# Performance work log

Hardware: AMD Instinct MI355X
Metric: run time of the kernel (lower is better)

## Reference

```python
import jax, jax.numpy as jnp
import numpy as np

D_MODEL = 1024
NUM_HEADS = 16

def setup_inputs() -> dict:
    key = jax.random.key(0)
    ks = jax.random.split(key, 9)
    d = D_MODEL
    s = 0.02
    return {
        "x": jax.random.normal(ks[0], (2, 2048, d), dtype=jnp.float32),
        "wq": jax.random.normal(ks[1], (d, d), dtype=jnp.float32) * s,
        "bq": jax.random.normal(ks[2], (d,), dtype=jnp.float32) * s,
        "wk": jax.random.normal(ks[3], (d, d), dtype=jnp.float32) * s,
        "bk": jax.random.normal(ks[4], (d,), dtype=jnp.float32) * s,
        "wv": jax.random.normal(ks[5], (d, d), dtype=jnp.float32) * s,
        "bv": jax.random.normal(ks[6], (d,), dtype=jnp.float32) * s,
        "wo": jax.random.normal(ks[7], (d, d), dtype=jnp.float32) * s,
        "bo": jax.random.normal(ks[8], (d,), dtype=jnp.float32) * s,
    }

def reference(x, wq, bq, wk, bk, wv, bv, wo, bo) -> jnp.ndarray:
    b, s, d = x.shape
    h = NUM_HEADS
    dk = d // h
    # projections (torch Linear: x @ W^T + b)
    q = x @ wq.T + bq
    k = x @ wk.T + bk
    v = x @ wv.T + bv
    # split heads -> [b, h, s, dk]
    q = q.reshape(b, s, h, dk).transpose(0, 2, 1, 3)
    k = k.reshape(b, s, h, dk).transpose(0, 2, 1, 3)
    v = v.reshape(b, s, h, dk).transpose(0, 2, 1, 3)
    scale = jnp.sqrt(jnp.asarray(dk, dtype=x.dtype))
    scores = jnp.einsum('bhqd,bhkd->bhqk', q, k) / scale
    causal = jnp.tril(jnp.ones((s, s), dtype=bool))  # [s, s]
    scores = jnp.where(causal[None, None], scores, jnp.asarray(-jnp.inf, dtype=x.dtype))
    attn = jax.nn.softmax(scores, axis=-1)
    out = jnp.einsum('bhqk,bhkd->bhqd', attn, v)
    out = out.transpose(0, 2, 1, 3).reshape(b, s, d)
    return out @ wo.T + bo
```

## Files before the change

### kernel.cpp

```cpp
#include <hip/hip_runtime.h>

#define D_MODEL 1024
#define NHEAD   16
#define DK      64
#define BATCH   2
#define SEQ     2048
#define M_TOT   (BATCH*SEQ)

typedef unsigned short u16;
typedef unsigned int   u32;
typedef __attribute__((ext_vector_type(8))) __bf16 bf16x8;
typedef __attribute__((ext_vector_type(8))) u16   u16x8;
typedef __attribute__((ext_vector_type(4))) u16   u16x4;
typedef __attribute__((ext_vector_type(4))) float f32x4;

typedef const __attribute__((address_space(1))) u32* gas_ptr;
typedef __attribute__((address_space(3))) u32*       las_ptr;

__device__ __forceinline__ void gload16(const u16* g, u16* l) {
  __builtin_amdgcn_global_load_lds((gas_ptr)g, (las_ptr)l, 16, 0, 0);
}

__device__ __forceinline__ u16 bfc(float f) {
  union { __bf16 h; u16 u; } v; v.h = (__bf16)f; return v.u;
}

#define BAR() do { \
  __builtin_amdgcn_sched_barrier(0); \
  __builtin_amdgcn_s_barrier(); \
  __builtin_amdgcn_sched_barrier(0); \
} while (0)

__global__ void cvt_all(const float* __restrict__ x,
                        const float* __restrict__ wq, const float* __restrict__ wk,
                        const float* __restrict__ wv, const float* __restrict__ wo,
                        u16* __restrict__ xbf, u16* __restrict__ wbf) {
  const int y = blockIdx.y;
  const float* src;
  u16* dst;
  int n8;
  if (y == 0)      { src = x;  dst = xbf;                n8 = M_TOT * D_MODEL / 8; }
  else if (y == 1) { src = wq; dst = wbf;                n8 = 1024 * 1024 / 8; }
  else if (y == 2) { src = wk; dst = wbf + 1 * 1048576;  n8 = 1024 * 1024 / 8; }
  else if (y == 3) { src = wv; dst = wbf + 2 * 1048576;  n8 = 1024 * 1024 / 8; }
  else             { src = wo; dst = wbf + 3 * 1048576;  n8 = 1024 * 1024 / 8; }
  for (int i = blockIdx.x * blockDim.x + threadIdx.x; i < n8; i += gridDim.x * blockDim.x) {
    const float4* s = (const float4*)src + (size_t)i * 2;
    float4 a = s[0], b = s[1];
    u16x8 o;
    o[0]=bfc(a.x); o[1]=bfc(a.y); o[2]=bfc(a.z); o[3]=bfc(a.w);
    o[4]=bfc(b.x); o[5]=bfc(b.y); o[6]=bfc(b.z); o[7]=bfc(b.w);
    *((u16x8*)dst + i) = o;
  }
}

#define QSCALE 0.18033688011112042f

__global__ __launch_bounds__(256) void qkv_gemm(
    const u16* __restrict__ xbf, const u16* __restrict__ wbf,
    const float* __restrict__ bq, const float* __restrict__ bk, const float* __restrict__ bv,
    u16* __restrict__ qws, u16* __restrict__ kws, u16* __restrict__ vtws)
{
  __shared__ u16 la[2 * 128 * 32];
  __shared__ u16 lb[2 * 64 * 32];
  const int z     = blockIdx.z;
  const int nbase = blockIdx.x * 64;
  const int mbase = blockIdx.y * 128;
  const u16*  A    = xbf;
  const u16*  Bm   = wbf + (size_t)z * 1024 * 1024;
  const float* bias = (z == 0) ? bq : (z == 1) ? bk : bv;

  const int tid  = threadIdx.x;
  const int lane = tid & 63;
  const int wid  = tid >> 6;
  const int wr   = (wid >> 1) * 64, wc = (wid & 1) * 32;
  const int lr   = lane & 15, lg = lane >> 4;
  const int srow = tid >> 2;
  const int sc   = tid & 3;
  const int sdst = srow * 32 + sc * 8;
  const int ssrc = (sc ^ ((srow >> 1) & 3)) * 8;
  const int csw  = (lg ^ ((lr >> 1) & 3)) * 8;

  f32x4 acc[4][2];
  #pragma unroll
  for (int i = 0; i < 4; ++i) { acc[i][0] = (f32x4){0,0,0,0}; acc[i][1] = (f32x4){0,0,0,0}; }

  #define STAGEQ(u, bi) do { \
    const int k0_ = (u) * 32; \
    gload16(&A [(size_t)(mbase + srow)      * 1024 + k0_ + ssrc], &la[(bi)*4096 + sdst]); \
    gload16(&A [(size_t)(mbase + srow + 64) * 1024 + k0_ + ssrc], &la[(bi)*4096 + 64*32 + sdst]); \
    gload16(&Bm[(size_t)(nbase + srow)      * 1024 + k0_ + ssrc], &lb[(bi)*2048 + sdst]); \
  } while (0)

  STAGEQ(0, 0);
  STAGEQ(1, 1);
  for (int t = 0; t < 32; ++t) {
    if (t < 31) asm volatile("s_waitcnt vmcnt(3)" ::: "memory");
    else        asm volatile("s_waitcnt vmcnt(0)" ::: "memory");
    BAR();
    const int cb = (t & 1) * 4096, cbb = (t & 1) * 2048;
    bf16x8 af[4], bfr[2];
    #pragma unroll
    for (int i = 0; i < 4; ++i)
      af[i] = *(const bf16x8*)&la[cb + (wr + i*16 + lr)*32 + csw];
    #pragma unroll
    for (int j = 0; j < 2; ++j)
      bfr[j] = *(const bf16x8*)&lb[cbb + (wc + j*16 + lr)*32 + csw];
    #pragma unroll
    for (int i = 0; i < 4; ++i)
      #pragma unroll
      for (int j = 0; j < 2; ++j)
        acc[i][j] = __builtin_amdgcn_mfma_f32_16x16x32_bf16(af[i], bfr[j], acc[i][j], 0, 0, 0);
    BAR();
    if (t + 2 < 32) STAGEQ(t + 2, t & 1);
  }
  #undef STAGEQ

  #pragma unroll
  for (int i = 0; i < 4; ++i) {
    #pragma unroll
    for (int j = 0; j < 2; ++j) {
      int gn = nbase + wc + j*16 + lr;
      float bs = bias[gn];
      int h = gn >> 6, d = gn & 63;
      int gm0 = mbase + wr + i*16 + lg*4;
      int bb = gm0 >> 11, s0 = gm0 & 2047;
      if (z == 2) {
        u16x4 vk;
        #pragma unroll
        for (int r = 0; r < 4; ++r) vk[r] = bfc(acc[i][j][r] + bs);
        *(u16x4*)&vtws[(((size_t)(bb*NHEAD + h)) * DK + d) * SEQ + s0] = vk;
      } else {
        #pragma unroll
        for (int r = 0; r < 4; ++r) {
          float v = acc[i][j][r] + bs;
          if (z == 0) qws[(((size_t)(bb*NHEAD + h)) * SEQ + s0 + r) * DK + d] = bfc(v * QSCALE);
          else        kws[(((size_t)(bb*NHEAD + h)) * SEQ + s0 + r) * DK + d] = bfc(v);
        }
      }
    }
  }
}

__global__ __launch_bounds__(256) void out_gemm(
    const u16* __restrict__ ows, const u16* __restrict__ wobf,
    const float* __restrict__ bo, float* __restrict__ out)
{
  __shared__ u16 la[2 * 64 * 64];
  __shared__ u16 lb[2 * 64 * 64];
  const int nbase = blockIdx.x * 64;
  const int mbase = blockIdx.y * 64;
  const int tid  = threadIdx.x;
  const int lane = tid & 63;
  const int wid  = tid >> 6;
  const int wr   = (wid >> 1) * 32, wc = (wid & 1) * 32;
  const int lr   = lane & 15, lg = lane >> 4;
  const int srow = tid >> 3;
  const int sc   = tid & 7;
  const int sdst = srow * 64 + sc * 8;
  const int ssrc = (sc ^ (srow & 7)) * 8;
  const int lsw  = lr & 7;

  f32x4 acc[2][2];
  acc[0][0] = (f32x4){0,0,0,0}; acc[0][1] = (f32x4){0,0,0,0};
  acc[1][0] = (f32x4){0,0,0,0}; acc[1][1] = (f32x4){0,0,0,0};

  #define STAGEO(u, bi) do { \
    const int k0_ = (u) * 64; \
    gload16(&ows [(size_t)(mbase + srow)      * 1024 + k0_ + ssrc], &la[(bi)*4096 + sdst]); \
    gload16(&ows [(size_t)(mbase + srow + 32) * 1024 + k0_ + ssrc], &la[(bi)*4096 + 32*64 + sdst]); \
    gload16(&wobf[(size_t)(nbase + srow)      * 1024 + k0_ + ssrc], &lb[(bi)*4096 + sdst]); \
    gload16(&wobf[(size_t)(nbase + srow + 32) * 1024 + k0_ + ssrc], &lb[(bi)*4096 + 32*64 + sdst]); \
  } while (0)

  STAGEO(0, 0);
  STAGEO(1, 1);
  for (int t = 0; t < 16; ++t) {
    if (t < 15) asm volatile("s_waitcnt vmcnt(4)" ::: "memory");
    else        asm volatile("s_waitcnt vmcnt(0)" ::: "memory");
    BAR();
    const int cb = (t & 1) * 4096;
    bf16x8 af[2][2], bfr[2][2];
    #pragma unroll
    for (int kk = 0; kk < 2; ++kk) {
      #pragma unroll
      for (int i = 0; i < 2; ++i)
        af[i][kk] = *(const bf16x8*)&la[cb + (wr + i*16 + lr)*64 + (((kk*4 + lg) ^ lsw) * 8)];
      #pragma unroll
      for (int j = 0; j < 2; ++j)
        bfr[j][kk] = *(const bf16x8*)&lb[cb + (wc + j*16 + lr)*64 + (((kk*4 + lg) ^ lsw) * 8)];
    }
    #pragma unroll
    for (int kk = 0; kk < 2; ++kk)
      #pragma unroll
      for (int i = 0; i < 2; ++i)
        #pragma unroll
        for (int j = 0; j < 2; ++j)
          acc[i][j] = __builtin_amdgcn_mfma_f32_16x16x32_bf16(af[i][kk], bfr[j][kk], acc[i][j], 0, 0, 0);
    BAR();
    if (t + 2 < 16) STAGEO(t + 2, t & 1);
  }
  #undef STAGEO

  #pragma unroll
  for (int i = 0; i < 2; ++i) {
    #pragma unroll
    for (int j = 0; j < 2; ++j) {
      int gn = nbase + wc + j*16 + lr;
      float bs = bo[gn];
      #pragma unroll
      for (int r = 0; r < 4; ++r) {
        int gm = mbase + wr + i*16 + lg*4 + r;
        out[(size_t)gm * 1024 + gn] = acc[i][j][r] + bs;
      }
    }
  }
}

__global__ __launch_bounds__(256) void attn_kernel(
    const u16* __restrict__ qws, const u16* __restrict__ kws,
    const u16* __restrict__ vtws, u16* __restrict__ ows)
{
  __shared__ u16 kbuf[2 * 64 * 64];
  __shared__ u16 vbuf[2 * 64 * 64];
  __shared__ u16 pbuf[4 * 16 * 64];
  const int flat = blockIdx.x;
  const int r    = flat & 7;
  const int g    = flat >> 3;
  const int bh_l = g >> 5;
  const int qp   = g & 31;
  const int qt   = (bh_l & 1) ? qp : (31 - qp);
  const int bh   = r * 4 + bh_l;
  const int b = bh >> 4, h = bh & 15;
  const int tid = threadIdx.x, wid = tid >> 6, lane = tid & 63;
  const int lr = lane & 15, lg = lane >> 4;
  const u16* Q  = qws  + (size_t)(b * NHEAD + h) * SEQ * DK;
  const u16* K  = kws  + (size_t)(b * NHEAD + h) * SEQ * DK;
  const u16* Vt = vtws + (size_t)(b * NHEAD + h) * DK * SEQ;

  const int sr  = tid >> 3;
  const int sc8 = (tid & 7) * 8;
  const int c0s = ((tid & 7) ^ (sr & 7)) * 8;
  const int c1s = ((tid & 7) ^ ((sr + 32) & 7)) * 8;

  #define STAGE(u, bi) do { \
    const int kb_ = (u) * 64; \
    const int off_ = (bi) * 4096; \
    gload16(&K[(size_t)(kb_ + sr) * DK + c0s],        &kbuf[off_ + sr * 64 + sc8]); \
    gload16(&K[(size_t)(kb_ + sr + 32) * DK + c1s],   &kbuf[off_ + (sr + 32) * 64 + sc8]); \
    gload16(&Vt[(size_t)sr * SEQ + kb_ + c0s],        &vbuf[off_ + sr * 64 + sc8]); \
    gload16(&Vt[(size_t)(sr + 32) * SEQ + kb_ + c1s], &vbuf[off_ + (sr + 32) * 64 + sc8]); \
  } while (0)
  #define CH(m) ((((m)*4 + lg) ^ (lr & 7)) * 8)

  const int qbase  = qt * 64 + wid * 16;
  const int q_glob = qbase + lr;

  bf16x8 qf0 = *(const bf16x8*)&Q[(size_t)q_glob * DK + lg * 8];
  bf16x8 qf1 = *(const bf16x8*)&Q[(size_t)q_glob * DK + 32 + lg * 8];

  f32x4 oacc[4];
  #pragma unroll
  for (int t = 0; t < 4; ++t) oacc[t] = (f32x4){0.f, 0.f, 0.f, 0.f};
  float l_run = 0.f;

  STAGE(0, 0);
  if (qt >= 1) STAGE(1, 1);

  for (int t = 0; t <= qt; ++t) {
    if (t < qt) asm volatile("s_waitcnt vmcnt(4)" ::: "memory");
    else        asm volatile("s_waitcnt vmcnt(0)" ::: "memory");
    BAR();

    const int diag = (t == qt);
    const int nsub = diag ? (wid + 1) : 4;
    const int cb = (t & 1) * 4096;

    f32x4 sacc[4];
    __builtin_amdgcn_s_setprio(1);
    #pragma unroll
    for (int ts = 0; ts < 4; ++ts) {
      if (ts >= nsub) continue;
      bf16x8 kf0 = *(const bf16x8*)&kbuf[cb + (ts*16 + lr) * 64 + CH(0)];
      bf16x8 kf1 = *(const bf16x8*)&kbuf[cb + (ts*16 + lr) * 64 + CH(1)];
      f32x4 s0 = (f32x4){0.f, 0.f, 0.f, 0.f};
      s0 = __builtin_amdgcn_mfma_f32_16x16x32_bf16(kf0, qf0, s0, 0, 0, 0);
      s0 = __builtin_amdgcn_mfma_f32_16x16x32_bf16(kf1, qf1, s0, 0, 0, 0);
      sacc[ts] = s0;
    }
    __builtin_amdgcn_s_setprio(0);
    if (diag) {
      const int ts = wid;
      #pragma unroll
      for (int r2 = 0; r2 < 4; ++r2)
        if (lg * 4 + r2 > lr) sacc[ts][r2] = -1e30f;
    }
    #pragma unroll
    for (int ts = 0; ts < 4; ++ts) {
      if (ts >= nsub) continue;
      #pragma unroll
      for (int r2 = 0; r2 < 4; ++r2) {
        float p = __builtin_amdgcn_exp2f(sacc[ts][r2]);
        sacc[ts][r2] = p;
        l_run += p;
      }
    }

    #pragma unroll
    for (int ts = 0; ts < 4; ++ts) {
      u16x4 pk;
      if (ts < nsub) {
        pk[0] = bfc(sacc[ts][0]); pk[1] = bfc(sacc[ts][1]);
        pk[2] = bfc(sacc[ts][2]); pk[3] = bfc(sacc[ts][3]);
      } else {
        pk[0] = 0; pk[1] = 0; pk[2] = 0; pk[3] = 0;
      }
      const int pc = (((ts*2 + (lg >> 1)) ^ (lr & 7)) * 8) + (lg & 1) * 4;
      *(u16x4*)&pbuf[wid * 1024 + lr * 64 + pc] = pk;
    }
    asm volatile("s_waitcnt lgkmcnt(0)" ::: "memory");
    __builtin_amdgcn_sched_barrier(0);
    bf16x8 pf0 = *(const bf16x8*)&pbuf[wid * 1024 + lr * 64 + CH(0)];
    bf16x8 pf1 = *(const bf16x8*)&pbuf[wid * 1024 + lr * 64 + CH(1)];

    __builtin_amdgcn_s_setprio(1);
    #pragma unroll
    for (int td = 0; td < 4; ++td) {
      bf16x8 vf0 = *(const bf16x8*)&vbuf[cb + (td*16 + lr) * 64 + CH(0)];
      bf16x8 vf1 = *(const bf16x8*)&vbuf[cb + (td*16 + lr) * 64 + CH(1)];
      oacc[td] = __builtin_amdgcn_mfma_f32_16x16x32_bf16(vf0, pf0, oacc[td], 0, 0, 0);
      oacc[td] = __builtin_amdgcn_mfma_f32_16x16x32_bf16(vf1, pf1, oacc[td], 0, 0, 0);
    }
    __builtin_amdgcn_s_setprio(0);
    BAR();
    if (t + 2 <= qt) STAGE(t + 2, t & 1);
  }

  float l_tot = l_run;
  l_tot += __shfl_xor(l_tot, 16);
  l_tot += __shfl_xor(l_tot, 32);
  const float inv = 1.0f / l_tot;
  #pragma unroll
  for (int td = 0; td < 4; ++td) {
    u16x4 ok;
    #pragma unroll
    for (int r2 = 0; r2 < 4; ++r2) ok[r2] = bfc(oacc[td][r2] * inv);
    *(u16x4*)&ows[((size_t)(b * SEQ + q_glob)) * D_MODEL + h * DK + td*16 + lg*4] = ok;
  }
  #undef CH
  #undef STAGE
}

extern "C" void kernel_launch(void* const* d_in, const int* in_sizes, int n_in,
                              void* d_out, int out_size, void* d_ws, size_t ws_size,
                              hipStream_t stream) {
  const float* x  = (const float*)d_in[0];
  const float* wq = (const float*)d_in[1];
  const float* bq = (const float*)d_in[2];
  const float* wk = (const float*)d_in[3];
  const float* bk = (const float*)d_in[4];
  const float* wv = (const float*)d_in[5];
  const float* bv = (const float*)d_in[6];
  const float* wo = (const float*)d_in[7];
  const float* bo = (const float*)d_in[8];
  float* out = (float*)d_out;

  char* ws = (char*)d_ws;
  u16* qws  = (u16*)(ws + (size_t) 0 * (1 << 20));
  u16* kws  = (u16*)(ws + (size_t) 8 * (1 << 20));
  u16* vtws = (u16*)(ws + (size_t)16 * (1 << 20));
  u16* ows  = (u16*)(ws + (size_t)24 * (1 << 20));
  u16* xbf  = (u16*)(ws + (size_t)32 * (1 << 20));
  u16* wbf  = (u16*)(ws + (size_t)40 * (1 << 20));

  cvt_all<<<dim3(512, 5), 256, 0, stream>>>(x, wq, wk, wv, wo, xbf, wbf);

  qkv_gemm<<<dim3(1024 / 64, M_TOT / 128, 3), 256, 0, stream>>>(
      xbf, wbf, bq, bk, bv, qws, kws, vtws);

  attn_kernel<<<dim3(1024, 1, 1), 256, 0, stream>>>(qws, kws, vtws, ows);

  out_gemm<<<dim3(1024 / 64, M_TOT / 64), 256, 0, stream>>>(
      ows, wbf + (size_t)3 * 1024 * 1024, bo, out);
}
```

Before: 113.4 us.

## Shrink projection GEMM blocks to 64x64 with two waves and simpler double buffering

Both projection GEMMs now use 128-thread blocks computing 64x64 tiles, with each wave owning a 64x32 slab. The QKV GEMM grid doubles to 3072 blocks, and the output GEMM moves to BK=32 with 32 k-steps. The hand-tuned vmcnt waits and depth-2 prefetch are replaced by a simpler prefetch-next-then-syncthreads loop. The aim is more blocks and better occupancy, at the cost of more global traffic per FLOP in the QKV GEMM and loads that may not be fully waited on before __syncthreads.

```diff
diff --git a/kernel.cpp b/kernel.cpp
--- a/kernel.cpp
+++ b/kernel.cpp
@@ -56,16 +56,16 @@
 
 #define QSCALE 0.18033688011112042f
 
-__global__ __launch_bounds__(256) void qkv_gemm(
+__global__ __launch_bounds__(128) void qkv_gemm(
     const u16* __restrict__ xbf, const u16* __restrict__ wbf,
     const float* __restrict__ bq, const float* __restrict__ bk, const float* __restrict__ bv,
     u16* __restrict__ qws, u16* __restrict__ kws, u16* __restrict__ vtws)
 {
-  __shared__ u16 la[2 * 128 * 32];
+  __shared__ u16 la[2 * 64 * 32];
   __shared__ u16 lb[2 * 64 * 32];
   const int z     = blockIdx.z;
   const int nbase = blockIdx.x * 64;
-  const int mbase = blockIdx.y * 128;
+  const int mbase = blockIdx.y * 64;
   const u16*  A    = xbf;
   const u16*  Bm   = wbf + (size_t)z * 1024 * 1024;
   const float* bias = (z == 0) ? bq : (z == 1) ? bk : bv;
@@ -73,7 +73,7 @@
   const int tid  = threadIdx.x;
   const int lane = tid & 63;
   const int wid  = tid >> 6;
-  const int wr   = (wid >> 1) * 64, wc = (wid & 1) * 32;
+  const int wc   = wid * 32;
   const int lr   = lane & 15, lg = lane >> 4;
   const int srow = tid >> 2;
   const int sc   = tid & 3;
@@ -87,32 +87,32 @@
 
   #define STAGEQ(u, bi) do { \
     const int k0_ = (u) * 32; \
-    gload16(&A [(size_t)(mbase + srow)      * 1024 + k0_ + ssrc], &la[(bi)*4096 + sdst]); \
-    gload16(&A [(size_t)(mbase + srow + 64) * 1024 + k0_ + ssrc], &la[(bi)*4096 + 64*32 + sdst]); \
+    gload16(&A [(size_t)(mbase + srow)      * 1024 + k0_ + ssrc], &la[(bi)*2048 + sdst]); \
+    gload16(&A [(size_t)(mbase + srow + 32) * 1024 + k0_ + ssrc], &la[(bi)*2048 + 1024 + sdst]); \
     gload16(&Bm[(size_t)(nbase + srow)      * 1024 + k0_ + ssrc], &lb[(bi)*2048 + sdst]); \
+    gload16(&Bm[(size_t)(nbase + srow + 32) * 1024 + k0_ + ssrc], &lb[(bi)*2048 + 1024 + sdst]); \
   } while (0)
 
   STAGEQ(0, 0);
-  STAGEQ(1, 1);
+  __syncthreads();
+  int cur = 0;
   for (int t = 0; t < 32; ++t) {
-    if (t < 31) asm volatile("s_waitcnt vmcnt(3)" ::: "memory");
-    else        asm volatile("s_waitcnt vmcnt(0)" ::: "memory");
-    BAR();
-    const int cb = (t & 1) * 4096, cbb = (t & 1) * 2048;
+    if (t < 31) STAGEQ(t + 1, cur ^ 1);
+    const int cb = cur * 2048;
     bf16x8 af[4], bfr[2];
     #pragma unroll
     for (int i = 0; i < 4; ++i)
-      af[i] = *(const bf16x8*)&la[cb + (wr + i*16 + lr)*32 + csw];
+      af[i] = *(const bf16x8*)&la[cb + (i*16 + lr)*32 + csw];
     #pragma unroll
     for (int j = 0; j < 2; ++j)
-      bfr[j] = *(const bf16x8*)&lb[cbb + (wc + j*16 + lr)*32 + csw];
+      bfr[j] = *(const bf16x8*)&lb[cb + (wc + j*16 + lr)*32 + csw];
     #pragma unroll
     for (int i = 0; i < 4; ++i)
       #pragma unroll
       for (int j = 0; j < 2; ++j)
         acc[i][j] = __builtin_amdgcn_mfma_f32_16x16x32_bf16(af[i], bfr[j], acc[i][j], 0, 0, 0);
-    BAR();
-    if (t + 2 < 32) STAGEQ(t + 2, t & 1);
+    __syncthreads();
+    cur ^= 1;
   }
   #undef STAGEQ
 
@@ -123,7 +123,7 @@
       int gn = nbase + wc + j*16 + lr;
       float bs = bias[gn];
       int h = gn >> 6, d = gn & 63;
-      int gm0 = mbase + wr + i*16 + lg*4;
+      int gm0 = mbase + i*16 + lg*4;
       int bb = gm0 >> 11, s0 = gm0 & 2047;
       if (z == 2) {
         u16x4 vk;
@@ -142,75 +142,69 @@
   }
 }
 
-__global__ __launch_bounds__(256) void out_gemm(
+__global__ __launch_bounds__(128) void out_gemm(
     const u16* __restrict__ ows, const u16* __restrict__ wobf,
     const float* __restrict__ bo, float* __restrict__ out)
 {
-  __shared__ u16 la[2 * 64 * 64];
-  __shared__ u16 lb[2 * 64 * 64];
+  __shared__ u16 la[2 * 64 * 32];
+  __shared__ u16 lb[2 * 64 * 32];
   const int nbase = blockIdx.x * 64;
   const int mbase = blockIdx.y * 64;
   const int tid  = threadIdx.x;
   const int lane = tid & 63;
   const int wid  = tid >> 6;
-  const int wr   = (wid >> 1) * 32, wc = (wid & 1) * 32;
+  const int wc   = wid * 32;
   const int lr   = lane & 15, lg = lane >> 4;
-  const int srow = tid >> 3;
-  const int sc   = tid & 7;
-  const int sdst = srow * 64 + sc * 8;
-  const int ssrc = (sc ^ (srow & 7)) * 8;
-  const int lsw  = lr & 7;
-
-  f32x4 acc[2][2];
-  acc[0][0] = (f32x4){0,0,0,0}; acc[0][1] = (f32x4){0,0,0,0};
-  acc[1][0] = (f32x4){0,0,0,0}; acc[1][1] = (f32x4){0,0,0,0};
+  const int srow = tid >> 2;
+  const int sc   = tid & 3;
+  const int sdst = srow * 32 + sc * 8;
+  const int ssrc = (sc ^ ((srow >> 1) & 3)) * 8;
+  const int csw  = (lg ^ ((lr >> 1) & 3)) * 8;
+
+  f32x4 acc[4][2];
+  #pragma unroll
+  for (int i = 0; i < 4; ++i) { acc[i][0] = (f32x4){0,0,0,0}; acc[i][1] = (f32x4){0,0,0,0}; }
 
   #define STAGEO(u, bi) do { \
-    const int k0_ = (u) * 64; \
-    gload16(&ows [(size_t)(mbase + srow)      * 1024 + k0_ + ssrc], &la[(bi)*4096 + sdst]); \
-    gload16(&ows [(size_t)(mbase + srow + 32) * 1024 + k0_ + ssrc], &la[(bi)*4096 + 32*64 + sdst]); \
-    gload16(&wobf[(size_t)(nbase + srow)      * 1024 + k0_ + ssrc], &lb[(bi)*4096 + sdst]); \
-    gload16(&wobf[(size_t)(nbase + srow + 32) * 1024 + k0_ + ssrc], &lb[(bi)*4096 + 32*64 + sdst]); \
+    const int k0_ = (u) * 32; \
+    gload16(&ows [(size_t)(mbase + srow)      * 1024 + k0_ + ssrc], &la[(bi)*2048 + sdst]); \
+    gload16(&ows [(size_t)(mbase + srow + 32) * 1024 + k0_ + ssrc], &la[(bi)*2048 + 1024 + sdst]); \
+    gload16(&wobf[(size_t)(nbase + srow)      * 1024 + k0_ + ssrc], &lb[(bi)*2048 + sdst]); \
+    gload16(&wobf[(size_t)(nbase + srow + 32) * 1024 + k0_ + ssrc], &lb[(bi)*2048 + 1024 + sdst]); \
   } while (0)
 
   STAGEO(0, 0);
-  STAGEO(1, 1);
-  for (int t = 0; t < 16; ++t) {
-    if (t < 15) asm volatile("s_waitcnt vmcnt(4)" ::: "memory");
-    else        asm volatile("s_waitcnt vmcnt(0)" ::: "memory");
-    BAR();
-    const int cb = (t & 1) * 4096;
-    bf16x8 af[2][2], bfr[2][2];
-    #pragma unroll
-    for (int kk = 0; kk < 2; ++kk) {
-      #pragma unroll
-      for (int i = 0; i < 2; ++i)
-        af[i][kk] = *(const bf16x8*)&la[cb + (wr + i*16 + lr)*64 + (((kk*4 + lg) ^ lsw) * 8)];
+  __syncthreads();
+  int cur = 0;
+  for (int t = 0; t < 32; ++t) {
+    if (t < 31) STAGEO(t + 1, cur ^ 1);
+    const int cb = cur * 2048;
+    bf16x8 af[4], bfr[2];
+    #pragma unroll
+    for (int i = 0; i < 4; ++i)
+      af[i] = *(const bf16x8*)&la[cb + (i*16 + lr)*32 + csw];
+    #pragma unroll
+    for (int j = 0; j < 2; ++j)
+      bfr[j] = *(const bf16x8*)&lb[cb + (wc + j*16 + lr)*32 + csw];
+    #pragma unroll
+    for (int i = 0; i < 4; ++i)
       #pragma unroll
       for (int j = 0; j < 2; ++j)
-        bfr[j][kk] = *(const bf16x8*)&lb[cb + (wc + j*16 + lr)*64 + (((kk*4 + lg) ^ lsw) * 8)];
-    }
-    #pragma unroll
-    for (int kk = 0; kk < 2; ++kk)
-      #pragma unroll
-      for (int i = 0; i < 2; ++i)
-        #pragma unroll
-        for (int j = 0; j < 2; ++j)
-          acc[i][j] = __builtin_amdgcn_mfma_f32_16x16x32_bf16(af[i][kk], bfr[j][kk], acc[i][j], 0, 0, 0);
-    BAR();
-    if (t + 2 < 16) STAGEO(t + 2, t & 1);
+        acc[i][j] = __builtin_amdgcn_mfma_f32_16x16x32_bf16(af[i], bfr[j], acc[i][j], 0, 0, 0);
+    __syncthreads();
+    cur ^= 1;
   }
   #undef STAGEO
 
   #pragma unroll
-  for (int i = 0; i < 2; ++i) {
+  for (int i = 0; i < 4; ++i) {
     #pragma unroll
     for (int j = 0; j < 2; ++j) {
       int gn = nbase + wc + j*16 + lr;
       float bs = bo[gn];
       #pragma unroll
       for (int r = 0; r < 4; ++r) {
-        int gm = mbase + wr + i*16 + lg*4 + r;
+        int gm = mbase + i*16 + lg*4 + r;
         out[(size_t)gm * 1024 + gn] = acc[i][j][r] + bs;
       }
     }
@@ -375,11 +369,11 @@
 
   cvt_all<<<dim3(512, 5), 256, 0, stream>>>(x, wq, wk, wv, wo, xbf, wbf);
 
-  qkv_gemm<<<dim3(1024 / 64, M_TOT / 128, 3), 256, 0, stream>>>(
+  qkv_gemm<<<dim3(16, 64, 3), 128, 0, stream>>>(
       xbf, wbf, bq, bk, bv, qws, kws, vtws);
 
   attn_kernel<<<dim3(1024, 1, 1), 256, 0, stream>>>(qws, kws, vtws, ows);
 
-  out_gemm<<<dim3(1024 / 64, M_TOT / 64), 256, 0, stream>>>(
+  out_gemm<<<dim3(16, 64), 128, 0, stream>>>(
       ows, wbf + (size_t)3 * 1024 * 1024, bo, out);
 }
```

Result: slower. 130.5 us (+15.0%).
